# Optimization experiments

Measured on AMD Instinct MI355X. Metric: run time of the kernel, lower is better.

## Reference

```python
import jax, jax.numpy as jnp
import numpy as np
from jax import lax

B, T, D, H = 128, 512, 512, 512
FORGET_BIAS = 1.0  # TF BasicLSTMCell default


def setup_inputs() -> dict:
    key = jax.random.key(0)
    k1, k2, k3 = jax.random.split(key, 3)
    scale = 1.0 / np.sqrt(D + H)
    return {
        "word_vectors": jax.random.normal(k1, (B, T, D), dtype=jnp.float32),
        "num_words": jax.random.randint(k2, (B,), 0, T, dtype=jnp.int32),
        "init_c": jnp.zeros((B, H), dtype=jnp.float32),
        "init_h": jnp.zeros((B, H), dtype=jnp.float32),
        "W": jax.random.normal(k3, (D + H, 4 * H), dtype=jnp.float32) * scale,  # gates i,j,f,o
        "b": jnp.zeros((4 * H,), dtype=jnp.float32),
    }


def reference(word_vectors, num_words, init_c, init_h, W, b):
    # word_vectors: [B, T, D] -> time-major [T, B, D]
    xs = jnp.transpose(word_vectors, (1, 0, 2))
    ts = jnp.arange(T, dtype=num_words.dtype)

    def step(carry, inp):
        c, h = carry
        x, t = inp
        z = jnp.concatenate([x, h], axis=-1) @ W + b  # [B, 4H]
        i, j, f, o = jnp.split(z, 4, axis=-1)  # TF gate order
        new_c = c * jax.nn.sigmoid(f + FORGET_BIAS) + jax.nn.sigmoid(i) * jnp.tanh(j)
        new_h = jnp.tanh(new_c) * jax.nn.sigmoid(o)
        mask = (t < num_words)[:, None]  # [B, 1]
        # static_rnn sequence_length semantics: copy state through, zero outputs
        c2 = jnp.where(mask, new_c, c)
        h2 = jnp.where(mask, new_h, h)
        out = jnp.where(mask, new_h, jnp.zeros_like(new_h))
        return (c2, h2), out

    (final_c, final_h), outputs = lax.scan(step, (init_c, init_h), (xs, ts))
    # outputs: [T, B, H] (time-major, like the list returned by static_rnn)
    return outputs, final_c, final_h
```

## Files before the change

kernel.cpp:

```cpp
#include <hip/hip_runtime.h>


#define B_ 128
#define T_ 512
#define D_ 512
#define H_ 512
#define POISON 0xFFFFFFFFu
#define POLL_CAP 8192

typedef __bf16 bf16x8 __attribute__((ext_vector_type(8)));
typedef float f32x4 __attribute__((ext_vector_type(4)));
typedef unsigned long long u64;

static __device__ __forceinline__ unsigned short f2bf(float f) {
  return __builtin_bit_cast(unsigned short, (__bf16)f);
}
static __device__ __forceinline__ float fast_sigmoid(float x) {
  return __builtin_amdgcn_rcpf(1.f + __expf(-x));
}
static __device__ __forceinline__ float fast_tanh(float x) {
  float xc = fminf(fmaxf(x, -15.f), 15.f);
  float t = __expf(-2.f * xc);
  return (1.f - t) * __builtin_amdgcn_rcpf(1.f + t);
}
static __device__ __forceinline__ bool clean64(u64 v) {
  return ((unsigned int)v != POISON) && ((unsigned int)(v >> 32) != POISON);
}

#define LBAR()                                             \
  do {                                                     \
    __asm__ volatile("s_waitcnt lgkmcnt(0)" ::: "memory"); \
    __builtin_amdgcn_s_barrier();                          \
    __asm__ volatile("" ::: "memory");                     \
  } while (0)

__global__ __launch_bounds__(256) void pack_w_kernel(const float* __restrict__ W,
                                                     unsigned short* __restrict__ Wp) {
  int tid = blockIdx.x * 256 + threadIdx.x;
  int j = tid & 7;
  int lane = (tid >> 3) & 63;
  int f = tid >> 9;
  int kt = f & 31;
  int w = (f >> 5) & 7;
  int hb = f >> 8;
  int k = (kt << 5) + ((lane >> 4) << 3) + j;
  int col = ((w & 3) << 9) + (hb << 5) + ((w >> 2) << 4) + (lane & 15);
  Wp[tid] = f2bf(W[k * 2048 + col]);
}

__global__ __launch_bounds__(1024) void init_ws_kernel(unsigned int* __restrict__ hg) {
  hg[blockIdx.x * 1024 + threadIdx.x] = POISON;
}

__global__ __launch_bounds__(512, 2) void lstm_persistent(
    const float* __restrict__ wv, const int* __restrict__ nw,
    const float* __restrict__ ic, const float* __restrict__ ih,
    const float* __restrict__ bias, const unsigned short* __restrict__ Wp,
    unsigned int* __restrict__ hg, float* __restrict__ out) {
  __shared__ __align__(16) unsigned short hlds[16 * 512];
  __shared__ __align__(16) unsigned short xlds[2][16 * 512];
  __shared__ float zbuf[8][16][17];

  const int tid = threadIdx.x;
  const int wgid = blockIdx.x;
  const int mg = wgid & 7;
  const int hb = wgid >> 3;
  const int w = tid >> 6;
  const int lane = tid & 63;
  const int g = w & 3;
  const int jj = w >> 2;

  const int er = tid >> 5;
  const int ec = tid & 31;
  const int grow = (mg << 4) + er;
  const int gcol = (hb << 5) + ec;

  const int nwv = nw[grow];
  float c_reg = ic[grow * H_ + gcol];
  float h_reg = ih[grow * H_ + gcol];

  uint4 wfrag[32];
  {
    const uint4* wp = (const uint4*)Wp + (size_t)((hb * 8 + w) * 32) * 64 + lane;
#pragma unroll
    for (int kt = 0; kt < 32; ++kt) wfrag[kt] = wp[kt * 64];
  }
  const float bv = bias[(g << 9) + (hb << 5) + (jj << 4) + (lane & 15)];

  auto slotp = [&](int s) { return hg + (size_t)(s * 8 + mg) * 4096; };

  const int hslot = (hb << 9) + ((er | ((ec >> 3) << 4)) << 3) + (ec & 7);

  auto publish_h = [&](unsigned int* dst) {
    unsigned int hv = (unsigned int)f2bf(h_reg);
    unsigned int up = (unsigned int)__shfl_down((int)hv, 1);
    if ((tid & 1) == 0)
      __hip_atomic_store(dst + (hslot >> 1), hv | (up << 16), __ATOMIC_RELAXED,
                         __HIP_MEMORY_SCOPE_AGENT);
  };

  auto wait_stage = [&](const unsigned int* slot) {
    const u64* s = (const u64*)slot;
    const u64* p0 = s + ((2 * w) << 7) + lane;
    const u64* p1 = p0 + 64;
    const u64* p2 = s + ((2 * w + 1) << 7) + lane;
    const u64* p3 = p2 + 64;
    u64 a0, a1, b0, b1;
    int it = 0;
    while (true) {
      a0 = __hip_atomic_load(p0, __ATOMIC_RELAXED, __HIP_MEMORY_SCOPE_AGENT);
      a1 = __hip_atomic_load(p1, __ATOMIC_RELAXED, __HIP_MEMORY_SCOPE_AGENT);
      b0 = __hip_atomic_load(p2, __ATOMIC_RELAXED, __HIP_MEMORY_SCOPE_AGENT);
      b1 = __hip_atomic_load(p3, __ATOMIC_RELAXED, __HIP_MEMORY_SCOPE_AGENT);
      if (__all(clean64(a0) && clean64(a1) && clean64(b0) && clean64(b1))) break;
      if (++it > POLL_CAP) break;
      if (it > 8) __builtin_amdgcn_s_sleep(1);
    }
    u64* d = (u64*)hlds;
    d[((2 * w) << 7) + lane] = a0;
    d[((2 * w) << 7) + 64 + lane] = a1;
    d[((2 * w + 1) << 7) + lane] = b0;
    d[((2 * w + 1) << 7) + 64 + lane] = b1;
  };

  auto repoison = [&](unsigned int* slot) {
    if (tid < 256)
      __hip_atomic_store(slot + (hb << 8) + tid, POISON, __ATOMIC_RELAXED,
                         __HIP_MEMORY_SCOPE_AGENT);
  };

  float4 xr[4];
  auto xissue = [&](int tt) {
    if (tt >= T_) return;
#pragma unroll
    for (int s2 = 0; s2 < 2; ++s2) {
      int e = tid + (s2 << 9);
      int ktx = e >> 6;
      int le = e & 63;
      int r = le & 15;
      int d = (ktx << 5) + ((le >> 4) << 3);
      const float* src = wv + ((size_t)((mg << 4) + r) * T_ + tt) * D_ + d;
      xr[2 * s2] = *(const float4*)src;
      xr[2 * s2 + 1] = *(const float4*)(src + 4);
    }
  };
  auto xcommit = [&](int buf, int tt) {
    if (tt >= T_) return;
#pragma unroll
    for (int s2 = 0; s2 < 2; ++s2) {
      int e = tid + (s2 << 9);
      int ktx = e >> 6;
      int le = e & 63;
      float4 xa = xr[2 * s2], xb = xr[2 * s2 + 1];
      bf16x8 v;
      v[0] = (__bf16)xa.x; v[1] = (__bf16)xa.y; v[2] = (__bf16)xa.z; v[3] = (__bf16)xa.w;
      v[4] = (__bf16)xb.x; v[5] = (__bf16)xb.y; v[6] = (__bf16)xb.z; v[7] = (__bf16)xb.w;
      *(bf16x8*)&xlds[buf][(ktx << 9) + (le << 3)] = v;
    }
  };

  f32x4 xA, xB;
  auto xpart = [&](int buf) {
    f32x4 A = {0.f, 0.f, 0.f, 0.f};
    f32x4 Bc = {0.f, 0.f, 0.f, 0.f};
#pragma unroll
    for (int kt = 0; kt < 8; ++kt) {
      bf16x8 a0 = *(const bf16x8*)&xlds[buf][(kt << 9) + (lane << 3)];
      bf16x8 a1 = *(const bf16x8*)&xlds[buf][((kt + 8) << 9) + (lane << 3)];
      A = __builtin_amdgcn_mfma_f32_16x16x32_bf16(
          a0, __builtin_bit_cast(bf16x8, wfrag[kt]), A, 0, 0, 0);
      Bc = __builtin_amdgcn_mfma_f32_16x16x32_bf16(
          a1, __builtin_bit_cast(bf16x8, wfrag[kt + 8]), Bc, 0, 0, 0);
    }
    xA = A;
    xB = Bc;
  };

  xissue(0); xcommit(0, 0);
  xissue(1); xcommit(1, 1);
#pragma unroll
  for (int s2 = 0; s2 < 2; ++s2) {
    int e = tid + (s2 << 9);
    int ktx = e >> 6;
    int le = e & 63;
    int r = le & 15;
    int d = (ktx << 5) + ((le >> 4) << 3);
    const float* src = ih + (size_t)((mg << 4) + r) * H_ + d;
    float4 ha = *(const float4*)src;
    float4 hbv = *(const float4*)(src + 4);
    bf16x8 v;
    v[0] = (__bf16)ha.x; v[1] = (__bf16)ha.y; v[2] = (__bf16)ha.z; v[3] = (__bf16)ha.w;
    v[4] = (__bf16)hbv.x; v[5] = (__bf16)hbv.y; v[6] = (__bf16)hbv.z; v[7] = (__bf16)hbv.w;
    *(bf16x8*)&hlds[(ktx << 9) + (le << 3)] = v;
  }
  __syncthreads();
  xpart(0);

  for (int t = 0; t < T_; ++t) {
    const int par = t & 1;
    unsigned int* hdst = slotp((t + 1) & 7);

    f32x4 c0 = xA, c1 = xB;
    f32x4 c2 = {0.f, 0.f, 0.f, 0.f};
    f32x4 c3 = {0.f, 0.f, 0.f, 0.f};
#pragma unroll
    for (int i = 0; i < 4; ++i) {
      bf16x8 a0 = *(const bf16x8*)&hlds[((4 * i) << 9) + (lane << 3)];
      bf16x8 a1 = *(const bf16x8*)&hlds[((4 * i + 1) << 9) + (lane << 3)];
      bf16x8 a2 = *(const bf16x8*)&hlds[((4 * i + 2) << 9) + (lane << 3)];
      bf16x8 a3 = *(const bf16x8*)&hlds[((4 * i + 3) << 9) + (lane << 3)];
      c0 = __builtin_amdgcn_mfma_f32_16x16x32_bf16(
          a0, __builtin_bit_cast(bf16x8, wfrag[16 + 4 * i]), c0, 0, 0, 0);
      c1 = __builtin_amdgcn_mfma_f32_16x16x32_bf16(
          a1, __builtin_bit_cast(bf16x8, wfrag[17 + 4 * i]), c1, 0, 0, 0);
      c2 = __builtin_amdgcn_mfma_f32_16x16x32_bf16(
          a2, __builtin_bit_cast(bf16x8, wfrag[18 + 4 * i]), c2, 0, 0, 0);
      c3 = __builtin_amdgcn_mfma_f32_16x16x32_bf16(
          a3, __builtin_bit_cast(bf16x8, wfrag[19 + 4 * i]), c3, 0, 0, 0);
    }
    {
      int q = lane >> 4, cl = lane & 15;
#pragma unroll
      for (int v = 0; v < 4; ++v)
        zbuf[w][q * 4 + v][cl] = (c0[v] + c1[v]) + (c2[v] + c3[v]) + bv;
    }
    LBAR();
    {
      int ej = ec >> 4, ecl = ec & 15;
      float zi = zbuf[ej * 4 + 0][er][ecl];
      float zj = zbuf[ej * 4 + 1][er][ecl];
      float zf = zbuf[ej * 4 + 2][er][ecl];
      float zo = zbuf[ej * 4 + 3][er][ecl];
      float si = fast_sigmoid(zi);
      float sf = fast_sigmoid(zf + 1.f);
      float so = fast_sigmoid(zo);
      float tj = fast_tanh(zj);
      float nc = c_reg * sf + si * tj;
      float nh = fast_tanh(nc) * so;
      bool m = t < nwv;
      c_reg = m ? nc : c_reg;
      h_reg = m ? nh : h_reg;
      publish_h(hdst);
      out[(size_t)t * (B_ * H_) + grow * H_ + gcol] = m ? nh : 0.f;
    }

    if (t + 1 < T_) {
      xissue(t + 2);
      xpart(1 - par);
      wait_stage(hdst);
      LBAR();
      repoison(slotp(t & 7));
      xcommit(par, t + 2);
    }
    if ((t & 3) == 3) __syncthreads(); else LBAR();
  }

  size_t base = (size_t)T_ * (B_ * H_);
  out[base + grow * H_ + gcol] = c_reg;
  out[base + B_ * H_ + grow * H_ + gcol] = h_reg;
}

extern "C" void kernel_launch(void* const* d_in, const int* in_sizes, int n_in,
                              void* d_out, int out_size, void* d_ws, size_t ws_size,
                              hipStream_t stream) {
  const float* wv = (const float*)d_in[0];
  const int* nw = (const int*)d_in[1];
  const float* ic = (const float*)d_in[2];
  const float* ih = (const float*)d_in[3];
  const float* W = (const float*)d_in[4];
  const float* bias = (const float*)d_in[5];
  float* out = (float*)d_out;

  char* ws = (char*)d_ws;
  unsigned short* Wp = (unsigned short*)ws;
  unsigned int* hg = (unsigned int*)(ws + (4u << 20));

  init_ws_kernel<<<256, 1024, 0, stream>>>(hg);
  pack_w_kernel<<<(1 << 21) / 256, 256, 0, stream>>>(W, Wp);
  lstm_persistent<<<128, 512, 0, stream>>>(wv, nw, ic, ih, bias, Wp, hg, out);
}
```

Baseline: 1.517 ms.

## Replace poison/repoison handshake with tagged 64-bit h exchange and register gate shuffles

Each published h pair now carries a timestep tag in the upper 32 bits, so waiters poll for a matching tag instead of non-poison values. This removes the repoison stores and one workgroup barrier per step and cuts the global ring from 8 slots to 2. The weight packing is remapped so each lane holds all four gates for its column, letting the zbuf LDS round trip and barrier be replaced by intra-wave xor shuffles. hlds is double-buffered to drop another barrier, at the cost of doubling polled traffic per step (64-bit tagged words) and relying on tag ordering for correctness.

```diff
diff --git a/kernel.cpp b/kernel.cpp
--- a/kernel.cpp
+++ b/kernel.cpp
@@ -5,7 +5,6 @@
 #define T_ 512
 #define D_ 512
 #define H_ 512
-#define POISON 0xFFFFFFFFu
 #define POLL_CAP 8192
 
 typedef __bf16 bf16x8 __attribute__((ext_vector_type(8)));
@@ -22,9 +21,6 @@
   float xc = fminf(fmaxf(x, -15.f), 15.f);
   float t = __expf(-2.f * xc);
   return (1.f - t) * __builtin_amdgcn_rcpf(1.f + t);
-}
-static __device__ __forceinline__ bool clean64(u64 v) {
-  return ((unsigned int)v != POISON) && ((unsigned int)(v >> 32) != POISON);
 }
 
 #define LBAR()                                             \
@@ -44,12 +40,13 @@
   int w = (f >> 5) & 7;
   int hb = f >> 8;
   int k = (kt << 5) + ((lane >> 4) << 3) + j;
-  int col = ((w & 3) << 9) + (hb << 5) + ((w >> 2) << 4) + (lane & 15);
+  int cb = lane & 15;
+  int col = ((cb >> 2) << 9) + (hb << 5) + (w << 2) + (cb & 3);
   Wp[tid] = f2bf(W[k * 2048 + col]);
 }
 
 __global__ __launch_bounds__(1024) void init_ws_kernel(unsigned int* __restrict__ hg) {
-  hg[blockIdx.x * 1024 + threadIdx.x] = POISON;
+  hg[blockIdx.x * 1024 + threadIdx.x] = 0u;
 }
 
 __global__ __launch_bounds__(512, 2) void lstm_persistent(
@@ -57,9 +54,8 @@
     const float* __restrict__ ic, const float* __restrict__ ih,
     const float* __restrict__ bias, const unsigned short* __restrict__ Wp,
     unsigned int* __restrict__ hg, float* __restrict__ out) {
-  __shared__ __align__(16) unsigned short hlds[16 * 512];
+  __shared__ __align__(16) unsigned short hlds[2][16 * 512];
   __shared__ __align__(16) unsigned short xlds[2][16 * 512];
-  __shared__ float zbuf[8][16][17];
 
   const int tid = threadIdx.x;
   const int wgid = blockIdx.x;
@@ -67,13 +63,14 @@
   const int hb = wgid >> 3;
   const int w = tid >> 6;
   const int lane = tid & 63;
-  const int g = w & 3;
-  const int jj = w >> 2;
-
-  const int er = tid >> 5;
-  const int ec = tid & 31;
+
+  const int q = lane >> 4;
+  const int gp = (lane >> 2) & 3;
+  const int hc = lane & 3;
+  const int er = (q << 2) + gp;
+  const int kin = (w << 2) | hc;
   const int grow = (mg << 4) + er;
-  const int gcol = (hb << 5) + ec;
+  const int gcol = (hb << 5) + kin;
 
   const int nwv = nw[grow];
   float c_reg = ic[grow * H_ + gcol];
@@ -85,48 +82,52 @@
 #pragma unroll
     for (int kt = 0; kt < 32; ++kt) wfrag[kt] = wp[kt * 64];
   }
-  const float bv = bias[(g << 9) + (hb << 5) + (jj << 4) + (lane & 15)];
-
-  auto slotp = [&](int s) { return hg + (size_t)(s * 8 + mg) * 4096; };
-
-  const int hslot = (hb << 9) + ((er | ((ec >> 3) << 4)) << 3) + (ec & 7);
-
-  auto publish_h = [&](unsigned int* dst) {
+  const float bv = bias[(gp << 9) + (hb << 5) + kin];
+
+  auto slot64 = [&](int s) { return (u64*)hg + (size_t)(s * 8 + mg) * 4096; };
+
+  const int hslot = (hb << 9) + ((er | ((kin >> 3) << 4)) << 3) + (kin & 7);
+  const int ppair = hslot >> 1;
+
+  auto publish_h = [&](u64* dst, unsigned int tag) {
     unsigned int hv = (unsigned int)f2bf(h_reg);
     unsigned int up = (unsigned int)__shfl_down((int)hv, 1);
-    if ((tid & 1) == 0)
-      __hip_atomic_store(dst + (hslot >> 1), hv | (up << 16), __ATOMIC_RELAXED,
+    if ((lane & 1) == 0) {
+      u64 vv = ((u64)tag << 32) | (u64)(hv | (up << 16));
+      __hip_atomic_store(dst + ppair, vv, __ATOMIC_RELAXED,
                          __HIP_MEMORY_SCOPE_AGENT);
-  };
-
-  auto wait_stage = [&](const unsigned int* slot) {
-    const u64* s = (const u64*)slot;
-    const u64* p0 = s + ((2 * w) << 7) + lane;
-    const u64* p1 = p0 + 64;
-    const u64* p2 = s + ((2 * w + 1) << 7) + lane;
-    const u64* p3 = p2 + 64;
-    u64 a0, a1, b0, b1;
+    }
+  };
+
+  auto wait_stage = [&](const u64* s, unsigned int want, unsigned short* dstlds) {
+    u64 v0, v1, v2, v3, v4, v5, v6, v7;
     int it = 0;
     while (true) {
-      a0 = __hip_atomic_load(p0, __ATOMIC_RELAXED, __HIP_MEMORY_SCOPE_AGENT);
-      a1 = __hip_atomic_load(p1, __ATOMIC_RELAXED, __HIP_MEMORY_SCOPE_AGENT);
-      b0 = __hip_atomic_load(p2, __ATOMIC_RELAXED, __HIP_MEMORY_SCOPE_AGENT);
-      b1 = __hip_atomic_load(p3, __ATOMIC_RELAXED, __HIP_MEMORY_SCOPE_AGENT);
-      if (__all(clean64(a0) && clean64(a1) && clean64(b0) && clean64(b1))) break;
+      v0 = __hip_atomic_load(s + (((2 * w + 0) << 8) + (0 << 6) + lane), __ATOMIC_RELAXED, __HIP_MEMORY_SCOPE_AGENT);
+      v1 = __hip_atomic_load(s + (((2 * w + 0) << 8) + (1 << 6) + lane), __ATOMIC_RELAXED, __HIP_MEMORY_SCOPE_AGENT);
+      v2 = __hip_atomic_load(s + (((2 * w + 0) << 8) + (2 << 6) + lane), __ATOMIC_RELAXED, __HIP_MEMORY_SCOPE_AGENT);
+      v3 = __hip_atomic_load(s + (((2 * w + 0) << 8) + (3 << 6) + lane), __ATOMIC_RELAXED, __HIP_MEMORY_SCOPE_AGENT);
+      v4 = __hip_atomic_load(s + (((2 * w + 1) << 8) + (0 << 6) + lane), __ATOMIC_RELAXED, __HIP_MEMORY_SCOPE_AGENT);
+      v5 = __hip_atomic_load(s + (((2 * w + 1) << 8) + (1 << 6) + lane), __ATOMIC_RELAXED, __HIP_MEMORY_SCOPE_AGENT);
+      v6 = __hip_atomic_load(s + (((2 * w + 1) << 8) + (2 << 6) + lane), __ATOMIC_RELAXED, __HIP_MEMORY_SCOPE_AGENT);
+      v7 = __hip_atomic_load(s + (((2 * w + 1) << 8) + (3 << 6) + lane), __ATOMIC_RELAXED, __HIP_MEMORY_SCOPE_AGENT);
+      bool ok = ((unsigned int)(v0 >> 32) == want) && ((unsigned int)(v1 >> 32) == want) &&
+                ((unsigned int)(v2 >> 32) == want) && ((unsigned int)(v3 >> 32) == want) &&
+                ((unsigned int)(v4 >> 32) == want) && ((unsigned int)(v5 >> 32) == want) &&
+                ((unsigned int)(v6 >> 32) == want) && ((unsigned int)(v7 >> 32) == want);
+      if (__all(ok)) break;
       if (++it > POLL_CAP) break;
-      if (it > 8) __builtin_amdgcn_s_sleep(1);
-    }
-    u64* d = (u64*)hlds;
-    d[((2 * w) << 7) + lane] = a0;
-    d[((2 * w) << 7) + 64 + lane] = a1;
-    d[((2 * w + 1) << 7) + lane] = b0;
-    d[((2 * w + 1) << 7) + 64 + lane] = b1;
-  };
-
-  auto repoison = [&](unsigned int* slot) {
-    if (tid < 256)
-      __hip_atomic_store(slot + (hb << 8) + tid, POISON, __ATOMIC_RELAXED,
-                         __HIP_MEMORY_SCOPE_AGENT);
+      if (it > 4) __builtin_amdgcn_s_sleep(1);
+    }
+    unsigned int* d32 = (unsigned int*)dstlds;
+    d32[((2 * w + 0) << 8) + (0 << 6) + lane] = (unsigned int)v0;
+    d32[((2 * w + 0) << 8) + (1 << 6) + lane] = (unsigned int)v1;
+    d32[((2 * w + 0) << 8) + (2 << 6) + lane] = (unsigned int)v2;
+    d32[((2 * w + 0) << 8) + (3 << 6) + lane] = (unsigned int)v3;
+    d32[((2 * w + 1) << 8) + (0 << 6) + lane] = (unsigned int)v4;
+    d32[((2 * w + 1) << 8) + (1 << 6) + lane] = (unsigned int)v5;
+    d32[((2 * w + 1) << 8) + (2 << 6) + lane] = (unsigned int)v6;
+    d32[((2 * w + 1) << 8) + (3 << 6) + lane] = (unsigned int)v7;
   };
 
   float4 xr[4];
@@ -191,24 +192,25 @@
     bf16x8 v;
     v[0] = (__bf16)ha.x; v[1] = (__bf16)ha.y; v[2] = (__bf16)ha.z; v[3] = (__bf16)ha.w;
     v[4] = (__bf16)hbv.x; v[5] = (__bf16)hbv.y; v[6] = (__bf16)hbv.z; v[7] = (__bf16)hbv.w;
-    *(bf16x8*)&hlds[(ktx << 9) + (le << 3)] = v;
+    *(bf16x8*)&hlds[0][(ktx << 9) + (le << 3)] = v;
   }
   __syncthreads();
   xpart(0);
 
   for (int t = 0; t < T_; ++t) {
     const int par = t & 1;
-    unsigned int* hdst = slotp((t + 1) & 7);
-
+    u64* hdst = slot64((t + 1) & 1);
+
+    const unsigned short* hsrc = hlds[par];
     f32x4 c0 = xA, c1 = xB;
     f32x4 c2 = {0.f, 0.f, 0.f, 0.f};
     f32x4 c3 = {0.f, 0.f, 0.f, 0.f};
 #pragma unroll
     for (int i = 0; i < 4; ++i) {
-      bf16x8 a0 = *(const bf16x8*)&hlds[((4 * i) << 9) + (lane << 3)];
-      bf16x8 a1 = *(const bf16x8*)&hlds[((4 * i + 1) << 9) + (lane << 3)];
-      bf16x8 a2 = *(const bf16x8*)&hlds[((4 * i + 2) << 9) + (lane << 3)];
-      bf16x8 a3 = *(const bf16x8*)&hlds[((4 * i + 3) << 9) + (lane << 3)];
+      bf16x8 a0 = *(const bf16x8*)&hsrc[((4 * i) << 9) + (lane << 3)];
+      bf16x8 a1 = *(const bf16x8*)&hsrc[((4 * i + 1) << 9) + (lane << 3)];
+      bf16x8 a2 = *(const bf16x8*)&hsrc[((4 * i + 2) << 9) + (lane << 3)];
+      bf16x8 a3 = *(const bf16x8*)&hsrc[((4 * i + 3) << 9) + (lane << 3)];
       c0 = __builtin_amdgcn_mfma_f32_16x16x32_bf16(
           a0, __builtin_bit_cast(bf16x8, wfrag[16 + 4 * i]), c0, 0, 0, 0);
       c1 = __builtin_amdgcn_mfma_f32_16x16x32_bf16(
@@ -218,41 +220,41 @@
       c3 = __builtin_amdgcn_mfma_f32_16x16x32_bf16(
           a3, __builtin_bit_cast(bf16x8, wfrag[19 + 4 * i]), c3, 0, 0, 0);
     }
+
+    float z0 = (c0[0] + c1[0]) + (c2[0] + c3[0]) + bv;
+    float z1 = (c0[1] + c1[1]) + (c2[1] + c3[1]) + bv;
+    float z2 = (c0[2] + c1[2]) + (c2[2] + c3[2]) + bv;
+    float z3 = (c0[3] + c1[3]) + (c2[3] + c3[3]) + bv;
     {
-      int q = lane >> 4, cl = lane & 15;
-#pragma unroll
-      for (int v = 0; v < 4; ++v)
-        zbuf[w][q * 4 + v][cl] = (c0[v] + c1[v]) + (c2[v] + c3[v]) + bv;
-    }
-    LBAR();
+      bool b0 = gp & 1;
+      float e;
+      e = __shfl_xor(b0 ? z0 : z1, 4); if (b0) z0 = e; else z1 = e;
+      e = __shfl_xor(b0 ? z2 : z3, 4); if (b0) z2 = e; else z3 = e;
+      bool b1 = (gp >> 1) & 1;
+      e = __shfl_xor(b1 ? z0 : z2, 8); if (b1) z0 = e; else z2 = e;
+      e = __shfl_xor(b1 ? z1 : z3, 8); if (b1) z1 = e; else z3 = e;
+    }
     {
-      int ej = ec >> 4, ecl = ec & 15;
-      float zi = zbuf[ej * 4 + 0][er][ecl];
-      float zj = zbuf[ej * 4 + 1][er][ecl];
-      float zf = zbuf[ej * 4 + 2][er][ecl];
-      float zo = zbuf[ej * 4 + 3][er][ecl];
-      float si = fast_sigmoid(zi);
-      float sf = fast_sigmoid(zf + 1.f);
-      float so = fast_sigmoid(zo);
-      float tj = fast_tanh(zj);
+      float si = fast_sigmoid(z0);
+      float tj = fast_tanh(z1);
+      float sf = fast_sigmoid(z2 + 1.f);
+      float so = fast_sigmoid(z3);
       float nc = c_reg * sf + si * tj;
       float nh = fast_tanh(nc) * so;
       bool m = t < nwv;
       c_reg = m ? nc : c_reg;
       h_reg = m ? nh : h_reg;
-      publish_h(hdst);
+      publish_h(hdst, (unsigned int)(t + 1));
       out[(size_t)t * (B_ * H_) + grow * H_ + gcol] = m ? nh : 0.f;
     }
 
     if (t + 1 < T_) {
       xissue(t + 2);
       xpart(1 - par);
-      wait_stage(hdst);
-      LBAR();
-      repoison(slotp(t & 7));
+      wait_stage(hdst, (unsigned int)(t + 1), hlds[par ^ 1]);
       xcommit(par, t + 2);
     }
-    if ((t & 3) == 3) __syncthreads(); else LBAR();
+    LBAR();
   }
 
   size_t base = (size_t)T_ * (B_ * H_);
@@ -275,7 +277,7 @@
   unsigned short* Wp = (unsigned short*)ws;
   unsigned int* hg = (unsigned int*)(ws + (4u << 20));
 
-  init_ws_kernel<<<256, 1024, 0, stream>>>(hg);
+  init_ws_kernel<<<128, 1024, 0, stream>>>(hg);
   pack_w_kernel<<<(1 << 21) / 256, 256, 0, stream>>>(W, Wp);
   lstm_persistent<<<128, 512, 0, stream>>>(wv, nw, ic, ih, bias, Wp, hg, out);
 }
```

After: 1.719 ms. +13.3%, slower.
